# Kernel optimization log

Hardware: AMD Instinct MI355X
Metric: run time of the kernel (lower is better)

Reference implementation:

```python
import jax, jax.numpy as jnp
import numpy as np

N_NODES = 100000
Z_DIM = 64
N_EDGES = 1000000
H = 64

def setup_inputs() -> dict:
    key = jax.random.key(0)
    k1, k2, k3, k4 = jax.random.split(key, 4)
    z = jax.random.normal(k1, (N_NODES, Z_DIM), dtype=jnp.float32)
    edge = jax.random.randint(k2, (2, N_EDGES), 0, N_NODES, dtype=jnp.int64)
    # Linear params (stored as [in, out] for x @ W + b)
    W1 = jax.random.normal(k3, (2 * Z_DIM, H), dtype=jnp.float32) * (1.0 / np.sqrt(2 * Z_DIM))
    b1 = jnp.zeros((H,), dtype=jnp.float32)
    W2 = jax.random.normal(k4, (H, 1), dtype=jnp.float32) * (1.0 / np.sqrt(H))
    b2 = jnp.zeros((1,), dtype=jnp.float32)
    return {"z": z, "edge": edge, "W1": W1, "b1": b1, "W2": W2, "b2": b2}

def reference(z, edge, W1, b1, W2, b2):
    zi = z[edge[0]]                      # [E, z_dim] gather
    zj = z[edge[1]]                      # [E, z_dim] gather
    h = jnp.concatenate([zi, zj], axis=-1)  # [E, 2*z_dim]
    h = jax.nn.relu(h @ W1 + b1)         # [E, H]
    out = h @ W2 + b2                    # [E, 1]
    return out.squeeze(-1)               # [E]
```

## Files before the change

kernel.cpp:

```cpp
#include <hip/hip_runtime.h>
#include <hip/hip_bf16.h>

typedef unsigned short u16;
typedef unsigned int u32;
typedef __attribute__((ext_vector_type(8))) short bf16x8;
typedef __attribute__((ext_vector_type(16))) float f32x16;
typedef _Float16 h16x2 __attribute__((ext_vector_type(2)));

static __device__ __forceinline__ u16 f2bf(float f) {
    __hip_bfloat16 b = __float2bfloat16(f);
    return *(u16*)&b;
}
static __device__ __forceinline__ u16 f2h(float f) {
    _Float16 h = (_Float16)f;
    return __builtin_bit_cast(u16, h);
}

__global__ __launch_bounds__(256) void build_wfrag(
    const float* __restrict__ W1, u16* __restrict__ wtab)
{
    const int flat = blockIdx.x * 256 + threadIdx.x;
    if (flat >= 8192) return;
    const int j    = flat & 7;
    const int lane = (flat >> 3) & 63;
    const int ks   = (flat >> 9) & 3;
    const int ct   = flat >> 11;
    const int k = ks * 16 + (lane >> 5) * 8 + j;
    const int c = ct * 32 + (lane & 31);
    const float v = (c < 64) ? W1[(size_t)k * 64 + c]
                             : W1[(size_t)(64 + k) * 64 + (c - 64)];
    wtab[flat] = f2bf(v);
}

__global__ __launch_bounds__(256) void node_mfma(
    const float* __restrict__ z, const u16* __restrict__ wtab,
    const float* __restrict__ b1, u16* __restrict__ pq, int nNodes)
{
    const int lane   = threadIdx.x & 63;
    const int wave   = threadIdx.x >> 6;
    const int l31    = lane & 31;
    const int half   = lane >> 5;
    const int nodeBase = (blockIdx.x * 4 + wave) * 32;
    if (nodeBase >= nNodes) return;

    const bf16x8* wt = (const bf16x8*)wtab;
    bf16x8 Bf[4][4];
#pragma unroll
    for (int ct = 0; ct < 4; ++ct)
#pragma unroll
        for (int ks = 0; ks < 4; ++ks)
            Bf[ct][ks] = wt[(ct * 4 + ks) * 64 + lane];

    int zrowi = nodeBase + l31;
    if (zrowi > nNodes - 1) zrowi = nNodes - 1;
    const float* zrow = z + (size_t)zrowi * 64;
    bf16x8 Af[4];
#pragma unroll
    for (int ks = 0; ks < 4; ++ks) {
        const float4 v0 = *(const float4*)(zrow + ks * 16 + half * 8);
        const float4 v1 = *(const float4*)(zrow + ks * 16 + half * 8 + 4);
        Af[ks][0] = (short)f2bf(v0.x); Af[ks][1] = (short)f2bf(v0.y);
        Af[ks][2] = (short)f2bf(v0.z); Af[ks][3] = (short)f2bf(v0.w);
        Af[ks][4] = (short)f2bf(v1.x); Af[ks][5] = (short)f2bf(v1.y);
        Af[ks][6] = (short)f2bf(v1.z); Af[ks][7] = (short)f2bf(v1.w);
    }

    f32x16 acc[4];
#pragma unroll
    for (int ct = 0; ct < 4; ++ct) acc[ct] = (f32x16)(0.0f);
#pragma unroll
    for (int ks = 0; ks < 4; ++ks)
#pragma unroll
        for (int ct = 0; ct < 4; ++ct)
            acc[ct] = __builtin_amdgcn_mfma_f32_32x32x16_bf16(
                Af[ks], Bf[ct][ks], acc[ct], 0, 0, 0);

#pragma unroll
    for (int ct = 0; ct < 4; ++ct) {
        const int c = ct * 32 + l31;
        const float bias = (c < 64) ? b1[c] : 0.0f;
#pragma unroll
        for (int reg = 0; reg < 16; ++reg) {
            const int r = (reg & 3) + 8 * (reg >> 2) + 4 * half;
            const int node = nodeBase + r;
            if (node < nNodes)
                pq[(size_t)node * 128 + c] = f2h(acc[ct][reg] + bias);
        }
    }
}

__global__ __launch_bounds__(256) void edge_mlp(
    const int* __restrict__ e0, const int* __restrict__ e1,
    const u16* __restrict__ pq, const float* __restrict__ W2,
    const float* __restrict__ b2, float* __restrict__ out, int E)
{
    const int gid = blockIdx.x * 256 + threadIdx.x;
    const int e   = gid >> 3;
    const int sub = gid & 7;
    if (e >= E) return;

    const int i = e0[e];
    const int j = e1[e];

    const uint4 p = ((const uint4*)(pq + (size_t)i * 128))[sub];
    const uint4 q = ((const uint4*)(pq + (size_t)j * 128 + 64))[sub];

    const float4 wa = ((const float4*)W2)[2 * sub];
    const float4 wb = ((const float4*)W2)[2 * sub + 1];

    const u32 pw[4] = {p.x, p.y, p.z, p.w};
    const u32 qw[4] = {q.x, q.y, q.z, q.w};

    h16x2 w2h[4];
    w2h[0] = (h16x2){(_Float16)wa.x, (_Float16)wa.y};
    w2h[1] = (h16x2){(_Float16)wa.z, (_Float16)wa.w};
    w2h[2] = (h16x2){(_Float16)wb.x, (_Float16)wb.y};
    w2h[3] = (h16x2){(_Float16)wb.z, (_Float16)wb.w};
    const h16x2 hzero = (h16x2){(_Float16)0.0f, (_Float16)0.0f};

    float sum = 0.0f;
#pragma unroll
    for (int c = 0; c < 4; ++c) {
        h16x2 pp = __builtin_bit_cast(h16x2, pw[c]);
        h16x2 qq = __builtin_bit_cast(h16x2, qw[c]);
        h16x2 a  = __builtin_elementwise_max(pp + qq, hzero);
#if __has_builtin(__builtin_amdgcn_fdot2)
        sum = __builtin_amdgcn_fdot2(a, w2h[c], sum, false);
#else
        sum = fmaf((float)a[0], (float)w2h[c][0],
              fmaf((float)a[1], (float)w2h[c][1], sum));
#endif
    }

    sum += __shfl_xor(sum, 1);
    sum += __shfl_xor(sum, 2);
    sum += __shfl_xor(sum, 4);

    if (sub == 0) out[e] = sum + b2[0];
}

extern "C" void kernel_launch(void* const* d_in, const int* in_sizes, int n_in,
                              void* d_out, int out_size, void* d_ws, size_t ws_size,
                              hipStream_t stream) {
    const float* z  = (const float*)d_in[0];
    const int*   eg = (const int*)d_in[1];
    const float* W1 = (const float*)d_in[2];
    const float* b1 = (const float*)d_in[3];
    const float* W2 = (const float*)d_in[4];
    const float* b2 = (const float*)d_in[5];
    float* out = (float*)d_out;

    const int nNodes = in_sizes[0] / 64;
    const int E      = in_sizes[1] / 2;

    u16* wtab = (u16*)d_ws;
    u16* pq   = (u16*)d_ws + 16384;

    build_wfrag<<<dim3(32), dim3(256), 0, stream>>>(W1, wtab);

    dim3 gA((nNodes + 127) / 128);
    node_mfma<<<gA, dim3(256), 0, stream>>>(z, wtab, b1, pq, nNodes);

    long long tB = (long long)E * 8;
    dim3 gB((unsigned)((tB + 255) / 256));
    edge_mlp<<<gB, dim3(256), 0, stream>>>(eg, eg + E, pq, W2, b2, out, E);
}
```

Before: 122.8 us.

## Stage node outputs through swizzled LDS for coalesced stores; widen edge per-thread loads

The node kernel swaps the MFMA operands so each lane holds contiguous output columns, and seeds the accumulator with the bias. It packs the results to fp16 into a per-wave XOR-swizzled shared-memory tile, then writes each node row with 16-byte coalesced stores instead of scattered 2-byte stores. The edge kernel uses 4 threads per edge with two 16-byte loads each and one fewer shuffle step. W2 is pre-converted to fp16 in the setup kernel. This adds 32 KB of shared memory per block, which may limit occupancy.

```diff
diff --git a/kernel.cpp b/kernel.cpp
--- a/kernel.cpp
+++ b/kernel.cpp
@@ -5,6 +5,7 @@
 typedef unsigned int u32;
 typedef __attribute__((ext_vector_type(8))) short bf16x8;
 typedef __attribute__((ext_vector_type(16))) float f32x16;
+typedef __attribute__((ext_vector_type(2))) unsigned int u32x2;
 typedef _Float16 h16x2 __attribute__((ext_vector_type(2)));
 
 static __device__ __forceinline__ u16 f2bf(float f) {
@@ -17,19 +18,23 @@
 }
 
 __global__ __launch_bounds__(256) void build_wfrag(
-    const float* __restrict__ W1, u16* __restrict__ wtab)
+    const float* __restrict__ W1, const float* __restrict__ W2,
+    u16* __restrict__ wtab)
 {
     const int flat = blockIdx.x * 256 + threadIdx.x;
-    if (flat >= 8192) return;
-    const int j    = flat & 7;
-    const int lane = (flat >> 3) & 63;
-    const int ks   = (flat >> 9) & 3;
-    const int ct   = flat >> 11;
-    const int k = ks * 16 + (lane >> 5) * 8 + j;
-    const int c = ct * 32 + (lane & 31);
-    const float v = (c < 64) ? W1[(size_t)k * 64 + c]
-                             : W1[(size_t)(64 + k) * 64 + (c - 64)];
-    wtab[flat] = f2bf(v);
+    if (flat < 8192) {
+        const int j    = flat & 7;
+        const int lane = (flat >> 3) & 63;
+        const int ks   = (flat >> 9) & 3;
+        const int ct   = flat >> 11;
+        const int k = ks * 16 + (lane >> 5) * 8 + j;
+        const int c = ct * 32 + (lane & 31);
+        const float v = (c < 64) ? W1[(size_t)k * 64 + c]
+                                 : W1[(size_t)(64 + k) * 64 + (c - 64)];
+        wtab[flat] = f2bf(v);
+    } else if (flat < 8256) {
+        wtab[flat] = f2h(W2[flat - 8192]);
+    }
 }
 
 __global__ __launch_bounds__(256) void node_mfma(
@@ -43,98 +48,119 @@
     const int nodeBase = (blockIdx.x * 4 + wave) * 32;
     if (nodeBase >= nNodes) return;
 
+    __shared__ u16 tile[4][4096];
+
     const bf16x8* wt = (const bf16x8*)wtab;
-    bf16x8 Bf[4][4];
+    bf16x8 Wf[4][4];
 #pragma unroll
     for (int ct = 0; ct < 4; ++ct)
 #pragma unroll
         for (int ks = 0; ks < 4; ++ks)
-            Bf[ct][ks] = wt[(ct * 4 + ks) * 64 + lane];
+            Wf[ct][ks] = wt[(ct * 4 + ks) * 64 + lane];
 
     int zrowi = nodeBase + l31;
     if (zrowi > nNodes - 1) zrowi = nNodes - 1;
     const float* zrow = z + (size_t)zrowi * 64;
-    bf16x8 Af[4];
+    bf16x8 Zf[4];
 #pragma unroll
     for (int ks = 0; ks < 4; ++ks) {
         const float4 v0 = *(const float4*)(zrow + ks * 16 + half * 8);
         const float4 v1 = *(const float4*)(zrow + ks * 16 + half * 8 + 4);
-        Af[ks][0] = (short)f2bf(v0.x); Af[ks][1] = (short)f2bf(v0.y);
-        Af[ks][2] = (short)f2bf(v0.z); Af[ks][3] = (short)f2bf(v0.w);
-        Af[ks][4] = (short)f2bf(v1.x); Af[ks][5] = (short)f2bf(v1.y);
-        Af[ks][6] = (short)f2bf(v1.z); Af[ks][7] = (short)f2bf(v1.w);
+        Zf[ks][0] = (short)f2bf(v0.x); Zf[ks][1] = (short)f2bf(v0.y);
+        Zf[ks][2] = (short)f2bf(v0.z); Zf[ks][3] = (short)f2bf(v0.w);
+        Zf[ks][4] = (short)f2bf(v1.x); Zf[ks][5] = (short)f2bf(v1.y);
+        Zf[ks][6] = (short)f2bf(v1.z); Zf[ks][7] = (short)f2bf(v1.w);
     }
 
     f32x16 acc[4];
 #pragma unroll
-    for (int ct = 0; ct < 4; ++ct) acc[ct] = (f32x16)(0.0f);
+    for (int ct = 0; ct < 2; ++ct)
+#pragma unroll
+        for (int g = 0; g < 4; ++g) {
+            const float4 bv = *(const float4*)(b1 + ct * 32 + g * 8 + half * 4);
+            acc[ct][4 * g + 0] = bv.x; acc[ct][4 * g + 1] = bv.y;
+            acc[ct][4 * g + 2] = bv.z; acc[ct][4 * g + 3] = bv.w;
+        }
+    acc[2] = (f32x16)(0.0f);
+    acc[3] = (f32x16)(0.0f);
+
 #pragma unroll
     for (int ks = 0; ks < 4; ++ks)
 #pragma unroll
         for (int ct = 0; ct < 4; ++ct)
             acc[ct] = __builtin_amdgcn_mfma_f32_32x32x16_bf16(
-                Af[ks], Bf[ct][ks], acc[ct], 0, 0, 0);
+                Wf[ct][ks], Zf[ks], acc[ct], 0, 0, 0);
+
+    char* tb = (char*)&tile[wave][0];
+#pragma unroll
+    for (int ct = 0; ct < 4; ++ct)
+#pragma unroll
+        for (int g = 0; g < 4; ++g) {
+            const u32 lo = (u32)f2h(acc[ct][4 * g + 0]) |
+                           ((u32)f2h(acc[ct][4 * g + 1]) << 16);
+            const u32 hi = (u32)f2h(acc[ct][4 * g + 2]) |
+                           ((u32)f2h(acc[ct][4 * g + 3]) << 16);
+            const int roff = (ct * 64 + g * 16 + half * 8) ^ ((l31 & 7) << 4);
+            *(u32x2*)(tb + l31 * 256 + roff) = (u32x2){lo, hi};
+        }
 
 #pragma unroll
-    for (int ct = 0; ct < 4; ++ct) {
-        const int c = ct * 32 + l31;
-        const float bias = (c < 64) ? b1[c] : 0.0f;
-#pragma unroll
-        for (int reg = 0; reg < 16; ++reg) {
-            const int r = (reg & 3) + 8 * (reg >> 2) + 4 * half;
-            const int node = nodeBase + r;
-            if (node < nNodes)
-                pq[(size_t)node * 128 + c] = f2h(acc[ct][reg] + bias);
-        }
+    for (int it = 0; it < 8; ++it) {
+        const int c16  = lane + 64 * it;
+        const int nd   = c16 >> 4;
+        const int roff = ((c16 & 15) * 16) ^ ((nd & 7) << 4);
+        const uint4 v = *(const uint4*)(tb + nd * 256 + roff);
+        if (nodeBase + nd < nNodes)
+            *(uint4*)(pq + (size_t)nodeBase * 128 + (size_t)c16 * 8) = v;
     }
 }
 
 __global__ __launch_bounds__(256) void edge_mlp(
     const int* __restrict__ e0, const int* __restrict__ e1,
-    const u16* __restrict__ pq, const float* __restrict__ W2,
+    const u16* __restrict__ pq, const u16* __restrict__ w2tab,
     const float* __restrict__ b2, float* __restrict__ out, int E)
 {
     const int gid = blockIdx.x * 256 + threadIdx.x;
-    const int e   = gid >> 3;
-    const int sub = gid & 7;
+    const int e   = gid >> 2;
+    const int sub = gid & 3;
     if (e >= E) return;
 
     const int i = e0[e];
     const int j = e1[e];
 
-    const uint4 p = ((const uint4*)(pq + (size_t)i * 128))[sub];
-    const uint4 q = ((const uint4*)(pq + (size_t)j * 128 + 64))[sub];
+    const uint4* pr = (const uint4*)(pq + (size_t)i * 128);
+    const uint4* qr = (const uint4*)(pq + (size_t)j * 128 + 64);
+    const uint4 p0 = pr[2 * sub];
+    const uint4 p1 = pr[2 * sub + 1];
+    const uint4 q0 = qr[2 * sub];
+    const uint4 q1 = qr[2 * sub + 1];
 
-    const float4 wa = ((const float4*)W2)[2 * sub];
-    const float4 wb = ((const float4*)W2)[2 * sub + 1];
+    const uint4* wr = (const uint4*)w2tab;
+    const uint4 w0 = wr[2 * sub];
+    const uint4 w1 = wr[2 * sub + 1];
 
-    const u32 pw[4] = {p.x, p.y, p.z, p.w};
-    const u32 qw[4] = {q.x, q.y, q.z, q.w};
-
-    h16x2 w2h[4];
-    w2h[0] = (h16x2){(_Float16)wa.x, (_Float16)wa.y};
-    w2h[1] = (h16x2){(_Float16)wa.z, (_Float16)wa.w};
-    w2h[2] = (h16x2){(_Float16)wb.x, (_Float16)wb.y};
-    w2h[3] = (h16x2){(_Float16)wb.z, (_Float16)wb.w};
+    const u32 pw[8] = {p0.x, p0.y, p0.z, p0.w, p1.x, p1.y, p1.z, p1.w};
+    const u32 qw[8] = {q0.x, q0.y, q0.z, q0.w, q1.x, q1.y, q1.z, q1.w};
+    const u32 ww[8] = {w0.x, w0.y, w0.z, w0.w, w1.x, w1.y, w1.z, w1.w};
     const h16x2 hzero = (h16x2){(_Float16)0.0f, (_Float16)0.0f};
 
     float sum = 0.0f;
 #pragma unroll
-    for (int c = 0; c < 4; ++c) {
+    for (int c = 0; c < 8; ++c) {
         h16x2 pp = __builtin_bit_cast(h16x2, pw[c]);
         h16x2 qq = __builtin_bit_cast(h16x2, qw[c]);
+        h16x2 wc = __builtin_bit_cast(h16x2, ww[c]);
         h16x2 a  = __builtin_elementwise_max(pp + qq, hzero);
 #if __has_builtin(__builtin_amdgcn_fdot2)
-        sum = __builtin_amdgcn_fdot2(a, w2h[c], sum, false);
+        sum = __builtin_amdgcn_fdot2(a, wc, sum, false);
 #else
-        sum = fmaf((float)a[0], (float)w2h[c][0],
-              fmaf((float)a[1], (float)w2h[c][1], sum));
+        sum = fmaf((float)a[0], (float)wc[0],
+              fmaf((float)a[1], (float)wc[1], sum));
 #endif
     }
 
     sum += __shfl_xor(sum, 1);
     sum += __shfl_xor(sum, 2);
-    sum += __shfl_xor(sum, 4);
 
     if (sub == 0) out[e] = sum + b2[0];
 }
@@ -156,12 +182,12 @@
     u16* wtab = (u16*)d_ws;
     u16* pq   = (u16*)d_ws + 16384;
 
-    build_wfrag<<<dim3(32), dim3(256), 0, stream>>>(W1, wtab);
+    build_wfrag<<<dim3(33), dim3(256), 0, stream>>>(W1, W2, wtab);
 
     dim3 gA((nNodes + 127) / 128);
     node_mfma<<<gA, dim3(256), 0, stream>>>(z, wtab, b1, pq, nNodes);
 
-    long long tB = (long long)E * 8;
+    long long tB = (long long)E * 4;
     dim3 gB((unsigned)((tB + 255) / 256));
-    edge_mlp<<<gB, dim3(256), 0, stream>>>(eg, eg + E, pq, W2, b2, out, E);
+    edge_mlp<<<gB, dim3(256), 0, stream>>>(eg, eg + E, pq, wtab + 8192, b2, out, E);
 }
```

Result: no change. 122.7 us (-0.1%).
